# Performance work log

Measured on AMD Instinct MI355X. Metric: run time of the kernel, lower is better.

The kernel has to match this reference:

```python
import jax, jax.numpy as jnp
import numpy as np

N_NODES = 10000
D = 256


def setup_inputs() -> dict:
    key = jax.random.key(0)
    ks = jax.random.split(key, 16)
    x = jax.random.normal(ks[0], (N_NODES, D), dtype=jnp.float32)
    edge_index = jax.random.randint(ks[1], (2, 320000), 0, N_NODES, dtype=jnp.int64)

    def lin(k, din, dout, scale=None):
        s = scale if scale is not None else 1.0 / np.sqrt(din)
        return jax.random.uniform(k, (dout, din), dtype=jnp.float32, minval=-s, maxval=s)

    # SAGEConv: lin_l (neighbors, with bias), lin_r (root, no bias)
    W_l = lin(ks[2], D, D)
    b_l = jnp.zeros((D,), dtype=jnp.float32)
    W_r = lin(ks[3], D, D)
    # MLP stack
    Wa, ba = lin(ks[4], 256, 128), jax.random.uniform(ks[5], (128,), minval=-1/16, maxval=1/16)
    W1, b1 = lin(ks[6], 128, 64), jax.random.uniform(ks[7], (64,), minval=-np.sqrt(1/128), maxval=np.sqrt(1/128))
    W2, b2 = lin(ks[8], 64, 32), jax.random.uniform(ks[9], (32,), minval=-0.125, maxval=0.125)
    W3, b3 = lin(ks[10], 32, 3), jax.random.uniform(ks[11], (3,), minval=-np.sqrt(1/32), maxval=np.sqrt(1/32))
    return {"x": x, "edge_index": edge_index,
            "W_l": W_l, "b_l": b_l, "W_r": W_r,
            "Wa": Wa, "ba": ba, "W1": W1, "b1": b1,
            "W2": W2, "b2": b2, "W3": W3, "b3": b3}


def reference(x, edge_index, W_l, b_l, W_r, Wa, ba, W1, b1, W2, b2, W3, b3):
    src, dst = edge_index[0], edge_index[1]
    # mean aggregation of source features at destination nodes
    msg = x[src]                                              # [E, D] gather
    agg = jax.ops.segment_sum(msg, dst, num_segments=N_NODES)  # [N, D] scatter
    deg = jax.ops.segment_sum(jnp.ones_like(dst, dtype=x.dtype), dst, num_segments=N_NODES)
    agg = agg / jnp.maximum(deg, 1.0)[:, None]
    # SAGEConv: lin_l(agg) + lin_r(x)
    h = agg @ W_l.T + b_l + x @ W_r.T
    h = jax.nn.relu(h)
    h = jax.nn.relu(h @ Wa.T + ba)
    h = jax.nn.relu(h @ W1.T + b1)
    h = jax.nn.relu(h @ W2.T + b2)
    return h @ W3.T + b3
```

## Files before the change

kernel.cpp:

```cpp
#include <hip/hip_runtime.h>

#define D 256
#define CAP 96
#define POISON 0xAAAAAAAAu

typedef _Float16 half8 __attribute__((ext_vector_type(8)));
typedef _Float16 half4 __attribute__((ext_vector_type(4)));
typedef _Float16 half2v __attribute__((ext_vector_type(2)));
typedef float f32x4 __attribute__((ext_vector_type(4)));


__global__ __launch_bounds__(256) void prep_kernel(
    const float* __restrict__ x, const float* __restrict__ W_l,
    const float* __restrict__ W_r, const float* __restrict__ Wa,
    const int* __restrict__ src, const int* __restrict__ dst,
    _Float16* __restrict__ A, _Float16* __restrict__ B,
    _Float16* __restrict__ Wa16,
    int* __restrict__ cnt, int* __restrict__ csr,
    int total8, int E, int bX, int bW, int bWa) {
    const int b = blockIdx.x;
    const int t = threadIdx.x;
    if (b < bX) {
        int i = b * 256 + t;
        if (i >= total8) return;
        int m = i >> 5;
        int c = (i & 31) << 3;
        float4 v0 = *(const float4*)&x[(long)m * 256 + c];
        float4 v1 = *(const float4*)&x[(long)m * 256 + c + 4];
        half8 h = {(_Float16)v0.x, (_Float16)v0.y, (_Float16)v0.z, (_Float16)v0.w,
                   (_Float16)v1.x, (_Float16)v1.y, (_Float16)v1.z, (_Float16)v1.w};
        *(half8*)&A[(long)m * 512 + 256 + c] = h;
    } else if (b < bW) {
        int i = (b - bX) * 256 + t;
        int n = i >> 7;
        int k4 = (i & 127) << 2;
        float4 v = (k4 < 256) ? *(const float4*)&W_l[(long)n * 256 + k4]
                              : *(const float4*)&W_r[(long)n * 256 + (k4 - 256)];
        half4 h = {(_Float16)v.x, (_Float16)v.y, (_Float16)v.z, (_Float16)v.w};
        *(half4*)&B[(long)n * 512 + k4] = h;
    } else if (b < bWa) {
        int i = (b - bW) * 256 + t;
        int c = i << 2;
        float4 v = *(const float4*)&Wa[c];
        half4 h = {(_Float16)v.x, (_Float16)v.y, (_Float16)v.z, (_Float16)v.w};
        *(half4*)&Wa16[c] = h;
    } else {
        int e = (b - bWa) * 256 + t;
        if (e < E) {
            int d = dst[e];
            unsigned ret = (unsigned)atomicAdd(&cnt[d], 1);
            unsigned slot = ret - POISON;
            if (slot < CAP) csr[d * CAP + slot] = src[e];
        }
    }
}


__global__ __launch_bounds__(256) void agg_kernel(const int* __restrict__ csr,
                                                  const int* __restrict__ cnts,
                                                  _Float16* __restrict__ A, int M) {
    int node = (blockIdx.x * 256 + threadIdx.x) >> 6;
    int lane = threadIdx.x & 63;
    if (node >= M) return;
    int cnt = (int)((unsigned)cnts[node] - POISON);
    if (cnt > CAP) cnt = CAP;
    if (cnt < 0) cnt = 0;
    const int* row = csr + node * CAP;
    const int half = lane >> 5;
    const int hl   = lane & 31;
    const _Float16* xb = A + 256 + hl * 8;
    float acc[8] = {};
    int e = half;
    for (; e + 6 < cnt; e += 8) {
        int s0 = row[e], s1 = row[e + 2], s2 = row[e + 4], s3 = row[e + 6];
        half8 v0 = *(const half8*)(xb + (long)s0 * 512);
        half8 v1 = *(const half8*)(xb + (long)s1 * 512);
        half8 v2 = *(const half8*)(xb + (long)s2 * 512);
        half8 v3 = *(const half8*)(xb + (long)s3 * 512);
#pragma unroll
        for (int i = 0; i < 8; ++i)
            acc[i] += ((float)v0[i] + (float)v1[i]) + ((float)v2[i] + (float)v3[i]);
    }
    for (; e < cnt; e += 2) {
        int s = row[e];
        half8 v = *(const half8*)(xb + (long)s * 512);
#pragma unroll
        for (int i = 0; i < 8; ++i) acc[i] += (float)v[i];
    }
#pragma unroll
    for (int i = 0; i < 8; ++i) acc[i] += __shfl_down(acc[i], 32);
    if (half == 0) {
        float sc = 1.0f / (float)(cnt > 0 ? cnt : 1);
        half8 h;
#pragma unroll
        for (int i = 0; i < 8; ++i) h[i] = (_Float16)(acc[i] * sc);
        *(half8*)&A[(long)node * 512 + hl * 8] = h;
    }
}


template <int K, int NB, int WM>
__global__ __launch_bounds__(256) void gemm_mfma(const _Float16* __restrict__ A,
                                                 const _Float16* __restrict__ B,
                                                 const float* __restrict__ bias,
                                                 _Float16* __restrict__ Ch, int M) {
    constexpr int NC = K / 64;
    __shared__ __align__(16) _Float16 sB[2][64][72];

    const int tid  = threadIdx.x;
    const int wave = tid >> 6;
    const int lane = tid & 63;
    const int l16  = lane & 15;
    const int quad = lane >> 4;
    const int wr = wave % WM;
    const int cg = wave / WM;
    const int m_base = blockIdx.x * (WM * 16) + wr * 16;
    const int n0 = blockIdx.y * 64;

    int rowA = m_base + l16;
    if (rowA > M - 1) rowA = M - 1;
    const _Float16* pA = A + (long)rowA * K + quad * 8;

    auto stage = [&](int c) {
        const int buf = c & 1;
        const int kk = c * 64;
#pragma unroll
        for (int i = 0; i < 2; ++i) {
            int idx = tid + i * 256;
            int col = idx >> 3;
            int seg = (idx & 7) * 8;
            *(half8*)&sB[buf][col][seg] = *(const half8*)&B[(long)(n0 + col) * K + kk + seg];
        }
    };

    half8 a_reg[2][2];
    auto loadA = [&](int c) {
        const int buf = c & 1;
#pragma unroll
        for (int ks = 0; ks < 2; ++ks)
            a_reg[buf][ks] = *(const half8*)(pA + c * 64 + ks * 32);
    };

    f32x4 acc[WM] = {};

    stage(0);
    loadA(0);
    __syncthreads();
#pragma unroll
    for (int c = 0; c < NC; ++c) {
        if (c + 1 < NC) { stage(c + 1); loadA(c + 1); }
        const int buf = c & 1;
#pragma unroll
        for (int ks = 0; ks < 2; ++ks) {
            half8 a = a_reg[buf][ks];
#pragma unroll
            for (int t = 0; t < WM; ++t) {
                int col = cg * (WM * 16) + t * 16 + l16;
                half8 b = *(const half8*)&sB[buf][col][ks * 32 + quad * 8];
                acc[t] = __builtin_amdgcn_mfma_f32_16x16x32_f16(a, b, acc[t], 0, 0, 0);
            }
        }
        __syncthreads();
    }

#pragma unroll
    for (int t = 0; t < WM; ++t) {
        int n = n0 + cg * (WM * 16) + t * 16 + l16;
        float bv = bias[n];
#pragma unroll
        for (int r = 0; r < 4; ++r) {
            int m = m_base + quad * 4 + r;
            if (m < M) Ch[(long)m * NB + n] = (_Float16)fmaxf(acc[t][r] + bv, 0.f);
        }
    }
}


__global__ __launch_bounds__(512) void backend2345(
    const _Float16* __restrict__ h1, const _Float16* __restrict__ Wa16,
    const float* __restrict__ ba, const float* __restrict__ W1,
    const float* __restrict__ b1, const float* __restrict__ W2,
    const float* __restrict__ b2, const float* __restrict__ W3,
    const float* __restrict__ b3, float* __restrict__ out, int M) {
    __shared__ __align__(16) _Float16 sH1[32][264];
    __shared__ __align__(16) _Float16 sH2[32][136];
    __shared__ __align__(16) _Float16 sW1T[128][68];
    __shared__ __align__(16) _Float16 sW2T[64][40];
    __shared__ __align__(16) _Float16 sW3T[32][8];
    __shared__ __align__(16) _Float16 sH3[32][72];
    __shared__ __align__(16) _Float16 sH4[32][40];
    __shared__ float sb1[64], sb2[32], sb3[4];

    const int tid = threadIdx.x;
    const int r0 = blockIdx.x * 32;

#pragma unroll
    for (int it = 0; it < 2; ++it) {
        int i = tid + it * 512;
        int row = i >> 5;
        int c = (i & 31) << 3;
        half8 v = {};
        if (r0 + row < M) v = *(const half8*)&h1[(long)(r0 + row) * 256 + c];
        *(half8*)&sH1[row][c] = v;
    }
    for (int i = tid; i < 8192; i += 512) { int o = i >> 7, k = i & 127; sW1T[k][o] = (_Float16)W1[i]; }
    for (int i = tid; i < 2048; i += 512) { int o = i >> 6, k = i & 63;  sW2T[k][o] = (_Float16)W2[i]; }
    if (tid < 96) { int o = tid >> 5, k = tid & 31; sW3T[k][o] = (_Float16)W3[tid]; }
    if (tid < 64) sb1[tid] = b1[tid];
    else if (tid < 96) sb2[tid - 64] = b2[tid - 64];
    else if (tid < 100) sb3[tid - 96] = b3[tid - 96];
    __syncthreads();

    {
        const int wave = tid >> 6;
        const int lane = tid & 63;
        const int l16  = lane & 15;
        const int quad = lane >> 4;
        const int rbase = (wave & 1) * 16;
        const int cbase = (wave >> 1) * 32;

        const _Float16* pA = &sH1[rbase + l16][0] + quad * 8;

        f32x4 acc[2] = {};
#pragma unroll
        for (int c = 0; c < 8; ++c) {
            half8 a = *(const half8*)(pA + c * 32);
#pragma unroll
            for (int t = 0; t < 2; ++t) {
                int n = cbase + t * 16 + l16;
                half8 b = *(const half8*)&Wa16[(long)n * 256 + c * 32 + quad * 8];
                acc[t] = __builtin_amdgcn_mfma_f32_16x16x32_f16(a, b, acc[t], 0, 0, 0);
            }
        }
#pragma unroll
        for (int t = 0; t < 2; ++t) {
            int n = cbase + t * 16 + l16;
            float bv = ba[n];
#pragma unroll
            for (int r = 0; r < 4; ++r) {
                int ml = rbase + quad * 4 + r;
                sH2[ml][n] = (_Float16)fmaxf(acc[t][r] + bv, 0.f);
            }
        }
    }
    __syncthreads();

    const int r = tid >> 4;
    const int s = tid & 15;

    {
        float a0 = sb1[s * 4], a1 = sb1[s * 4 + 1], a2 = sb1[s * 4 + 2], a3 = sb1[s * 4 + 3];
        for (int k = 0; k < 128; k += 4) {
            half4 ah = *(const half4*)&sH2[r][k];
            float av[4] = {(float)ah[0], (float)ah[1], (float)ah[2], (float)ah[3]};
#pragma unroll
            for (int i = 0; i < 4; ++i) {
                half4 hw = *(const half4*)&sW1T[k + i][s * 4];
                a0 = fmaf(av[i], (float)hw[0], a0);
                a1 = fmaf(av[i], (float)hw[1], a1);
                a2 = fmaf(av[i], (float)hw[2], a2);
                a3 = fmaf(av[i], (float)hw[3], a3);
            }
        }
        half4 o = {(_Float16)fmaxf(a0, 0.f), (_Float16)fmaxf(a1, 0.f),
                   (_Float16)fmaxf(a2, 0.f), (_Float16)fmaxf(a3, 0.f)};
        *(half4*)&sH3[r][s * 4] = o;
    }
    __syncthreads();

    {
        float a0 = sb2[s * 2], a1 = sb2[s * 2 + 1];
        for (int k = 0; k < 64; k += 4) {
            half4 ah = *(const half4*)&sH3[r][k];
#pragma unroll
            for (int i = 0; i < 4; ++i) {
                half2v hw = *(const half2v*)&sW2T[k + i][s * 2];
                float av = (float)ah[i];
                a0 = fmaf(av, (float)hw[0], a0);
                a1 = fmaf(av, (float)hw[1], a1);
            }
        }
        half2v o = {(_Float16)fmaxf(a0, 0.f), (_Float16)fmaxf(a1, 0.f)};
        *(half2v*)&sH4[r][s * 2] = o;
    }
    __syncthreads();

    if (s < 3) {
        float acc = sb3[s];
        for (int k = 0; k < 32; k += 4) {
            half4 ah = *(const half4*)&sH4[r][k];
#pragma unroll
            for (int i = 0; i < 4; ++i)
                acc = fmaf((float)ah[i], (float)sW3T[k + i][s], acc);
        }
        if (r0 + r < M) out[(long)(r0 + r) * 3 + s] = acc;
    }
}


extern "C" void kernel_launch(void* const* d_in, const int* in_sizes, int n_in,
                              void* d_out, int out_size, void* d_ws, size_t ws_size,
                              hipStream_t stream) {
    const float* x   = (const float*)d_in[0];
    const int*   ei  = (const int*)d_in[1];
    const float* W_l = (const float*)d_in[2];
    const float* b_l = (const float*)d_in[3];
    const float* W_r = (const float*)d_in[4];
    const float* Wa  = (const float*)d_in[5];
    const float* ba  = (const float*)d_in[6];
    const float* W1  = (const float*)d_in[7];
    const float* b1  = (const float*)d_in[8];
    const float* W2  = (const float*)d_in[9];
    const float* b2  = (const float*)d_in[10];
    const float* W3  = (const float*)d_in[11];
    const float* b3  = (const float*)d_in[12];
    float* out = (float*)d_out;

    const int M = in_sizes[0] / D;
    const int E = in_sizes[1] / 2;
    const int* src = ei;
    const int* dst = ei + E;

    char* ws = (char*)d_ws;
    int*       cnt  = (int*)ws;       ws += 40064;
    int*       csr  = (int*)ws;       ws += (size_t)M * CAP * 4;
    _Float16*  A    = (_Float16*)ws;  ws += (size_t)M * 512 * 2;
    _Float16*  B    = (_Float16*)ws;  ws += (size_t)256 * 512 * 2;
    _Float16*  Wa16 = (_Float16*)ws;  ws += (size_t)128 * 256 * 2;
    _Float16*  h1   = (_Float16*)ws;  ws += (size_t)M * 256 * 2;

    const int total8 = M * 32;
    const int bX  = (total8 + 255) / 256;
    const int bW  = bX + 128;
    const int bWa = bW + 32;
    const int grid_prep = bWa + (E + 255) / 256;
    prep_kernel<<<grid_prep, 256, 0, stream>>>(x, W_l, W_r, Wa, src, dst, A, B, Wa16,
                                               cnt, csr, total8, E, bX, bW, bWa);

    agg_kernel<<<(M + 3) / 4, 256, 0, stream>>>(csr, cnt, A, M);

    gemm_mfma<512, 256, 4><<<dim3((M + 63) / 64, 4), 256, 0, stream>>>(
        A, B, b_l, h1, M);

    backend2345<<<(M + 31) / 32, 512, 0, stream>>>(
        h1, Wa16, ba, W1, b1, W2, b2, W3, b3, out, M);
}
```

Baseline: 155.1 us.

## Fuse neighbor aggregation, SAGE GEMM and MLP stack into one kernel

Replaces the separate aggregation, MFMA GEMM and MLP-backend kernels with a single kernel that works on 32 rows per block. Each block gathers neighbor means into LDS next to the root features, runs the 512-deep GEMM from LDS A and directly loaded B, and then runs the MLP layers in place. LDS buffers are shared through a union. This removes two launches and the global round trips of the concatenated A matrix and h1. In exchange, every block re-reads the full 256x512 weight matrix from global memory without LDS staging, and the gather is spread over fewer, larger blocks.

```diff
diff --git a/kernel.cpp b/kernel.cpp
--- a/kernel.cpp
+++ b/kernel.cpp
@@ -14,7 +14,7 @@
     const float* __restrict__ x, const float* __restrict__ W_l,
     const float* __restrict__ W_r, const float* __restrict__ Wa,
     const int* __restrict__ src, const int* __restrict__ dst,
-    _Float16* __restrict__ A, _Float16* __restrict__ B,
+    _Float16* __restrict__ X16, _Float16* __restrict__ B,
     _Float16* __restrict__ Wa16,
     int* __restrict__ cnt, int* __restrict__ csr,
     int total8, int E, int bX, int bW, int bWa) {
@@ -29,7 +29,7 @@
         float4 v1 = *(const float4*)&x[(long)m * 256 + c + 4];
         half8 h = {(_Float16)v0.x, (_Float16)v0.y, (_Float16)v0.z, (_Float16)v0.w,
                    (_Float16)v1.x, (_Float16)v1.y, (_Float16)v1.z, (_Float16)v1.w};
-        *(half8*)&A[(long)m * 512 + 256 + c] = h;
+        *(half8*)&X16[(long)m * 256 + c] = h;
     } else if (b < bW) {
         int i = (b - bX) * 256 + t;
         int n = i >> 7;
@@ -56,171 +56,132 @@
 }
 
 
-__global__ __launch_bounds__(256) void agg_kernel(const int* __restrict__ csr,
-                                                  const int* __restrict__ cnts,
-                                                  _Float16* __restrict__ A, int M) {
-    int node = (blockIdx.x * 256 + threadIdx.x) >> 6;
-    int lane = threadIdx.x & 63;
-    if (node >= M) return;
-    int cnt = (int)((unsigned)cnts[node] - POISON);
-    if (cnt > CAP) cnt = CAP;
-    if (cnt < 0) cnt = 0;
-    const int* row = csr + node * CAP;
-    const int half = lane >> 5;
-    const int hl   = lane & 31;
-    const _Float16* xb = A + 256 + hl * 8;
-    float acc[8] = {};
-    int e = half;
-    for (; e + 6 < cnt; e += 8) {
-        int s0 = row[e], s1 = row[e + 2], s2 = row[e + 4], s3 = row[e + 6];
-        half8 v0 = *(const half8*)(xb + (long)s0 * 512);
-        half8 v1 = *(const half8*)(xb + (long)s1 * 512);
-        half8 v2 = *(const half8*)(xb + (long)s2 * 512);
-        half8 v3 = *(const half8*)(xb + (long)s3 * 512);
-#pragma unroll
-        for (int i = 0; i < 8; ++i)
-            acc[i] += ((float)v0[i] + (float)v1[i]) + ((float)v2[i] + (float)v3[i]);
-    }
-    for (; e < cnt; e += 2) {
-        int s = row[e];
-        half8 v = *(const half8*)(xb + (long)s * 512);
-#pragma unroll
-        for (int i = 0; i < 8; ++i) acc[i] += (float)v[i];
-    }
-#pragma unroll
-    for (int i = 0; i < 8; ++i) acc[i] += __shfl_down(acc[i], 32);
-    if (half == 0) {
-        float sc = 1.0f / (float)(cnt > 0 ? cnt : 1);
-        half8 h;
-#pragma unroll
-        for (int i = 0; i < 8; ++i) h[i] = (_Float16)(acc[i] * sc);
-        *(half8*)&A[(long)node * 512 + hl * 8] = h;
-    }
-}
-
-
-template <int K, int NB, int WM>
-__global__ __launch_bounds__(256) void gemm_mfma(const _Float16* __restrict__ A,
-                                                 const _Float16* __restrict__ B,
-                                                 const float* __restrict__ bias,
-                                                 _Float16* __restrict__ Ch, int M) {
-    constexpr int NC = K / 64;
-    __shared__ __align__(16) _Float16 sB[2][64][72];
-
-    const int tid  = threadIdx.x;
-    const int wave = tid >> 6;
-    const int lane = tid & 63;
-    const int l16  = lane & 15;
-    const int quad = lane >> 4;
-    const int wr = wave % WM;
-    const int cg = wave / WM;
-    const int m_base = blockIdx.x * (WM * 16) + wr * 16;
-    const int n0 = blockIdx.y * 64;
-
-    int rowA = m_base + l16;
-    if (rowA > M - 1) rowA = M - 1;
-    const _Float16* pA = A + (long)rowA * K + quad * 8;
-
-    auto stage = [&](int c) {
-        const int buf = c & 1;
-        const int kk = c * 64;
-#pragma unroll
-        for (int i = 0; i < 2; ++i) {
-            int idx = tid + i * 256;
-            int col = idx >> 3;
-            int seg = (idx & 7) * 8;
-            *(half8*)&sB[buf][col][seg] = *(const half8*)&B[(long)(n0 + col) * K + kk + seg];
-        }
-    };
-
-    half8 a_reg[2][2];
-    auto loadA = [&](int c) {
-        const int buf = c & 1;
-#pragma unroll
-        for (int ks = 0; ks < 2; ++ks)
-            a_reg[buf][ks] = *(const half8*)(pA + c * 64 + ks * 32);
-    };
-
-    f32x4 acc[WM] = {};
-
-    stage(0);
-    loadA(0);
-    __syncthreads();
-#pragma unroll
-    for (int c = 0; c < NC; ++c) {
-        if (c + 1 < NC) { stage(c + 1); loadA(c + 1); }
-        const int buf = c & 1;
-#pragma unroll
-        for (int ks = 0; ks < 2; ++ks) {
-            half8 a = a_reg[buf][ks];
-#pragma unroll
-            for (int t = 0; t < WM; ++t) {
-                int col = cg * (WM * 16) + t * 16 + l16;
-                half8 b = *(const half8*)&sB[buf][col][ks * 32 + quad * 8];
-                acc[t] = __builtin_amdgcn_mfma_f32_16x16x32_f16(a, b, acc[t], 0, 0, 0);
-            }
-        }
-        __syncthreads();
-    }
-
-#pragma unroll
-    for (int t = 0; t < WM; ++t) {
-        int n = n0 + cg * (WM * 16) + t * 16 + l16;
-        float bv = bias[n];
-#pragma unroll
-        for (int r = 0; r < 4; ++r) {
-            int m = m_base + quad * 4 + r;
-            if (m < M) Ch[(long)m * NB + n] = (_Float16)fmaxf(acc[t][r] + bv, 0.f);
-        }
-    }
-}
-
-
-__global__ __launch_bounds__(512) void backend2345(
-    const _Float16* __restrict__ h1, const _Float16* __restrict__ Wa16,
-    const float* __restrict__ ba, const float* __restrict__ W1,
-    const float* __restrict__ b1, const float* __restrict__ W2,
-    const float* __restrict__ b2, const float* __restrict__ W3,
-    const float* __restrict__ b3, float* __restrict__ out, int M) {
+__global__ __launch_bounds__(512, 4) void fused_kernel(
+    const int* __restrict__ csr, const int* __restrict__ cnts,
+    const _Float16* __restrict__ X16, const _Float16* __restrict__ B,
+    const _Float16* __restrict__ Wa16,
+    const float* __restrict__ bl, const float* __restrict__ ba,
+    const float* __restrict__ W1, const float* __restrict__ b1,
+    const float* __restrict__ W2, const float* __restrict__ b2,
+    const float* __restrict__ W3, const float* __restrict__ b3,
+    float* __restrict__ out, int M) {
+    __shared__ __align__(16) union {
+        _Float16 sA[32][520];
+        struct {
+            _Float16 h2[32][136];
+            _Float16 h3[32][72];
+            _Float16 h4[32][40];
+        } s2;
+    } u;
     __shared__ __align__(16) _Float16 sH1[32][264];
-    __shared__ __align__(16) _Float16 sH2[32][136];
     __shared__ __align__(16) _Float16 sW1T[128][68];
     __shared__ __align__(16) _Float16 sW2T[64][40];
     __shared__ __align__(16) _Float16 sW3T[32][8];
-    __shared__ __align__(16) _Float16 sH3[32][72];
-    __shared__ __align__(16) _Float16 sH4[32][40];
-    __shared__ float sb1[64], sb2[32], sb3[4];
 
     const int tid = threadIdx.x;
     const int r0 = blockIdx.x * 32;
+    const int wave = tid >> 6;
+    const int lane = tid & 63;
+
+    for (int i = tid; i < 8192; i += 512) { int o = i >> 7, k = i & 127; sW1T[k][o] = (_Float16)W1[i]; }
+    for (int i = tid; i < 2048; i += 512) { int o = i >> 6, k = i & 63;  sW2T[k][o] = (_Float16)W2[i]; }
+    if (tid < 96) { int o = tid >> 5, k = tid & 31; sW3T[k][o] = (_Float16)W3[tid]; }
 
 #pragma unroll
     for (int it = 0; it < 2; ++it) {
         int i = tid + it * 512;
         int row = i >> 5;
         int c = (i & 31) << 3;
-        half8 v = {};
-        if (r0 + row < M) v = *(const half8*)&h1[(long)(r0 + row) * 256 + c];
-        *(half8*)&sH1[row][c] = v;
-    }
-    for (int i = tid; i < 8192; i += 512) { int o = i >> 7, k = i & 127; sW1T[k][o] = (_Float16)W1[i]; }
-    for (int i = tid; i < 2048; i += 512) { int o = i >> 6, k = i & 63;  sW2T[k][o] = (_Float16)W2[i]; }
-    if (tid < 96) { int o = tid >> 5, k = tid & 31; sW3T[k][o] = (_Float16)W3[tid]; }
-    if (tid < 64) sb1[tid] = b1[tid];
-    else if (tid < 96) sb2[tid - 64] = b2[tid - 64];
-    else if (tid < 100) sb3[tid - 96] = b3[tid - 96];
-    __syncthreads();
-
-    {
-        const int wave = tid >> 6;
-        const int lane = tid & 63;
+        int g = r0 + row;
+        if (g > M - 1) g = M - 1;
+        half8 v = *(const half8*)&X16[(long)g * 256 + c];
+        *(half8*)&u.sA[row][256 + c] = v;
+    }
+
+    {
+        const int half = lane >> 5;
+        const int hl   = lane & 31;
+        const _Float16* xb = X16 + hl * 8;
+#pragma unroll
+        for (int i = 0; i < 4; ++i) {
+            int row = wave * 4 + i;
+            int node = r0 + row;
+            int cnt = (int)((unsigned)cnts[node] - POISON);
+            if (cnt > CAP) cnt = CAP;
+            if (cnt < 0) cnt = 0;
+            const int* rowp = csr + (long)node * CAP;
+            float acc[8] = {};
+            int e = half;
+            for (; e + 6 < cnt; e += 8) {
+                int s0 = rowp[e], s1 = rowp[e + 2], s2 = rowp[e + 4], s3 = rowp[e + 6];
+                half8 v0 = *(const half8*)(xb + (long)s0 * 256);
+                half8 v1 = *(const half8*)(xb + (long)s1 * 256);
+                half8 v2 = *(const half8*)(xb + (long)s2 * 256);
+                half8 v3 = *(const half8*)(xb + (long)s3 * 256);
+#pragma unroll
+                for (int j = 0; j < 8; ++j)
+                    acc[j] += ((float)v0[j] + (float)v1[j]) + ((float)v2[j] + (float)v3[j]);
+            }
+            for (; e < cnt; e += 2) {
+                int s = rowp[e];
+                half8 v = *(const half8*)(xb + (long)s * 256);
+#pragma unroll
+                for (int j = 0; j < 8; ++j) acc[j] += (float)v[j];
+            }
+#pragma unroll
+            for (int j = 0; j < 8; ++j) acc[j] += __shfl_down(acc[j], 32);
+            if (half == 0) {
+                float sc = 1.0f / (float)(cnt > 0 ? cnt : 1);
+                half8 h;
+#pragma unroll
+                for (int j = 0; j < 8; ++j) h[j] = (_Float16)(acc[j] * sc);
+                *(half8*)&u.sA[row][hl * 8] = h;
+            }
+        }
+    }
+    __syncthreads();
+
+    {
+        const int l16  = lane & 15;
+        const int quad = lane >> 4;
+        const int nb = wave * 32;
+        const _Float16* pA0 = &u.sA[l16][0] + quad * 8;
+        const _Float16* pA1 = &u.sA[16 + l16][0] + quad * 8;
+        const _Float16* pB0 = B + (long)(nb + l16) * 512 + quad * 8;
+        const _Float16* pB1 = pB0 + 16 * 512;
+        f32x4 acc[2][2] = {};
+#pragma unroll
+        for (int c = 0; c < 16; ++c) {
+            half8 a0 = *(const half8*)(pA0 + c * 32);
+            half8 a1 = *(const half8*)(pA1 + c * 32);
+            half8 b0 = *(const half8*)(pB0 + c * 32);
+            half8 b1 = *(const half8*)(pB1 + c * 32);
+            acc[0][0] = __builtin_amdgcn_mfma_f32_16x16x32_f16(a0, b0, acc[0][0], 0, 0, 0);
+            acc[1][0] = __builtin_amdgcn_mfma_f32_16x16x32_f16(a1, b0, acc[1][0], 0, 0, 0);
+            acc[0][1] = __builtin_amdgcn_mfma_f32_16x16x32_f16(a0, b1, acc[0][1], 0, 0, 0);
+            acc[1][1] = __builtin_amdgcn_mfma_f32_16x16x32_f16(a1, b1, acc[1][1], 0, 0, 0);
+        }
+#pragma unroll
+        for (int nt = 0; nt < 2; ++nt) {
+            int n = nb + nt * 16 + l16;
+            float bv = bl[n];
+#pragma unroll
+            for (int mt = 0; mt < 2; ++mt)
+#pragma unroll
+                for (int r = 0; r < 4; ++r) {
+                    int m = mt * 16 + quad * 4 + r;
+                    sH1[m][n] = (_Float16)fmaxf(acc[mt][nt][r] + bv, 0.f);
+                }
+        }
+    }
+    __syncthreads();
+
+    {
         const int l16  = lane & 15;
         const int quad = lane >> 4;
         const int rbase = (wave & 1) * 16;
         const int cbase = (wave >> 1) * 32;
-
         const _Float16* pA = &sH1[rbase + l16][0] + quad * 8;
-
         f32x4 acc[2] = {};
 #pragma unroll
         for (int c = 0; c < 8; ++c) {
@@ -239,7 +200,7 @@
 #pragma unroll
             for (int r = 0; r < 4; ++r) {
                 int ml = rbase + quad * 4 + r;
-                sH2[ml][n] = (_Float16)fmaxf(acc[t][r] + bv, 0.f);
+                u.s2.h2[ml][n] = (_Float16)fmaxf(acc[t][r] + bv, 0.f);
             }
         }
     }
@@ -249,9 +210,9 @@
     const int s = tid & 15;
 
     {
-        float a0 = sb1[s * 4], a1 = sb1[s * 4 + 1], a2 = sb1[s * 4 + 2], a3 = sb1[s * 4 + 3];
+        float a0 = b1[s * 4], a1 = b1[s * 4 + 1], a2 = b1[s * 4 + 2], a3 = b1[s * 4 + 3];
         for (int k = 0; k < 128; k += 4) {
-            half4 ah = *(const half4*)&sH2[r][k];
+            half4 ah = *(const half4*)&u.s2.h2[r][k];
             float av[4] = {(float)ah[0], (float)ah[1], (float)ah[2], (float)ah[3]};
 #pragma unroll
             for (int i = 0; i < 4; ++i) {
@@ -264,14 +225,14 @@
         }
         half4 o = {(_Float16)fmaxf(a0, 0.f), (_Float16)fmaxf(a1, 0.f),
                    (_Float16)fmaxf(a2, 0.f), (_Float16)fmaxf(a3, 0.f)};
-        *(half4*)&sH3[r][s * 4] = o;
-    }
-    __syncthreads();
-
-    {
-        float a0 = sb2[s * 2], a1 = sb2[s * 2 + 1];
+        *(half4*)&u.s2.h3[r][s * 4] = o;
+    }
+    __syncthreads();
+
+    {
+        float a0 = b2[s * 2], a1 = b2[s * 2 + 1];
         for (int k = 0; k < 64; k += 4) {
-            half4 ah = *(const half4*)&sH3[r][k];
+            half4 ah = *(const half4*)&u.s2.h3[r][k];
 #pragma unroll
             for (int i = 0; i < 4; ++i) {
                 half2v hw = *(const half2v*)&sW2T[k + i][s * 2];
@@ -281,19 +242,19 @@
             }
         }
         half2v o = {(_Float16)fmaxf(a0, 0.f), (_Float16)fmaxf(a1, 0.f)};
-        *(half2v*)&sH4[r][s * 2] = o;
-    }
-    __syncthreads();
-
-    if (s < 3) {
-        float acc = sb3[s];
+        *(half2v*)&u.s2.h4[r][s * 2] = o;
+    }
+    __syncthreads();
+
+    if (s < 3 && r0 + r < M) {
+        float acc = b3[s];
         for (int k = 0; k < 32; k += 4) {
-            half4 ah = *(const half4*)&sH4[r][k];
+            half4 ah = *(const half4*)&u.s2.h4[r][k];
 #pragma unroll
             for (int i = 0; i < 4; ++i)
                 acc = fmaf((float)ah[i], (float)sW3T[k + i][s], acc);
         }
-        if (r0 + r < M) out[(long)(r0 + r) * 3 + s] = acc;
+        out[(long)(r0 + r) * 3 + s] = acc;
     }
 }
 
@@ -324,24 +285,18 @@
     char* ws = (char*)d_ws;
     int*       cnt  = (int*)ws;       ws += 40064;
     int*       csr  = (int*)ws;       ws += (size_t)M * CAP * 4;
-    _Float16*  A    = (_Float16*)ws;  ws += (size_t)M * 512 * 2;
+    _Float16*  X16  = (_Float16*)ws;  ws += (size_t)M * 256 * 2;
     _Float16*  B    = (_Float16*)ws;  ws += (size_t)256 * 512 * 2;
     _Float16*  Wa16 = (_Float16*)ws;  ws += (size_t)128 * 256 * 2;
-    _Float16*  h1   = (_Float16*)ws;  ws += (size_t)M * 256 * 2;
 
     const int total8 = M * 32;
     const int bX  = (total8 + 255) / 256;
     const int bW  = bX + 128;
     const int bWa = bW + 32;
     const int grid_prep = bWa + (E + 255) / 256;
-    prep_kernel<<<grid_prep, 256, 0, stream>>>(x, W_l, W_r, Wa, src, dst, A, B, Wa16,
+    prep_kernel<<<grid_prep, 256, 0, stream>>>(x, W_l, W_r, Wa, src, dst, X16, B, Wa16,
                                                cnt, csr, total8, E, bX, bW, bWa);
 
-    agg_kernel<<<(M + 3) / 4, 256, 0, stream>>>(csr, cnt, A, M);
-
-    gemm_mfma<512, 256, 4><<<dim3((M + 63) / 64, 4), 256, 0, stream>>>(
-        A, B, b_l, h1, M);
-
-    backend2345<<<(M + 31) / 32, 512, 0, stream>>>(
-        h1, Wa16, ba, W1, b1, W2, b2, W3, b3, out, M);
+    fused_kernel<<<(M + 31) / 32, 512, 0, stream>>>(
+        csr, cnt, X16, B, Wa16, b_l, ba, W1, b1, W2, b2, W3, b3, out, M);
 }
```

New measurement: 160.1 us. +3.2%, slower.
